# Kernel tuning notes

Measured on AMD Instinct MI355X. Metric: run time of the kernel, lower is better.

Reference implementation:

```python
import math
import jax, jax.numpy as jnp
import numpy as np

B, S, E = 2, 4096, 768
H, W = 12, 256  # num_heads, one-sided attention window
HD = E // H


def setup_inputs() -> dict:
    key = jax.random.key(0)
    ks = jax.random.split(key, 8)
    scale = 1.0 / math.sqrt(E)
    return {
        "hidden_states": jax.random.normal(ks[0], (B, S, E), jnp.float32),
        "attention_mask": jax.random.randint(ks[1], (B, 1, 1, S), 0, 2).astype(jnp.int32),
        "Wq": jax.random.normal(ks[2], (E, E), jnp.float32) * scale,
        "bq": jnp.zeros((E,), jnp.float32),
        "Wk": jax.random.normal(ks[3], (E, E), jnp.float32) * scale,
        "bk": jnp.zeros((E,), jnp.float32),
        "Wv": jax.random.normal(ks[4], (E, E), jnp.float32) * scale,
        "bv": jnp.zeros((E,), jnp.float32),
    }


def _to_heads(x, nc, w):
    # (B,S,E) -> (B*H, S, HD)
    return x.reshape(B, S, H, HD).transpose(0, 2, 1, 3).reshape(B * H, S, HD)


def _windows(x, nc, w):
    # (N, S, d) -> overlapping 3w key windows per query chunk: (N, nc, 3w, d)
    xp = jnp.pad(x, ((0, 0), (w, w), (0, 0))).reshape(x.shape[0], nc + 2, w, x.shape[-1])
    return jnp.concatenate([xp[:, :-2], xp[:, 1:-1], xp[:, 2:]], axis=2)


def reference(hidden_states, attention_mask, Wq, bq, Wk, bk, Wv, bv):
    w = W
    nc = S // w  # number of query chunks (seq_len % (2w) == 0)
    # Dense projections with relu activation (as in the source module)
    q = jax.nn.relu(hidden_states @ Wq + bq) / math.sqrt(HD)
    k = jax.nn.relu(hidden_states @ Wk + bk)
    v = jax.nn.relu(hidden_states @ Wv + bv)

    qc = _to_heads(q, nc, w).reshape(B * H, nc, w, HD)          # (BH, nc, w, d)
    kw = _windows(_to_heads(k, nc, w), nc, w)                    # (BH, nc, 3w, d)
    vw = _windows(_to_heads(v, nc, w), nc, w)                    # (BH, nc, 3w, d)

    # chunked QK^T: (BH, nc, w, 3w)
    scores = jnp.einsum('bcxd,bcyd->bcxy', qc, kw)

    rows = jnp.arange(w)[:, None]                                # (w,1)
    idx = rows + jnp.arange(2 * w + 1)[None, :]                  # (w, 2w+1) window column of diagonal j
    band = scores[:, :, rows, idx]                               # (BH, nc, w, 2w+1)

    # absolute key index of each band entry -> mask out-of-range diagonals
    abs_k = jnp.arange(nc)[:, None, None] * w + idx[None] - w    # (nc, w, 2w+1)
    valid = (abs_k >= 0) & (abs_k < S)

    # attention_mask != 0 -> add -10000 at those key positions within the band
    am = attention_mask.reshape(B, S)
    fm = jnp.where(am != 0, jnp.float32(-10000.0), jnp.float32(0.0))  # (B,S)
    fmp = jnp.pad(fm, ((0, 0), (w, w))).reshape(B, nc + 2, w)
    fmw = jnp.concatenate([fmp[:, :-2], fmp[:, 1:-1], fmp[:, 2:]], axis=2)  # (B, nc, 3w)
    fband = fmw[:, :, idx]                                       # (B, nc, w, 2w+1)

    band = band.reshape(B, H, nc, w, 2 * w + 1) + fband[:, None]
    band = jnp.where(valid, band, jnp.float32(-1e9))
    probs = jax.nn.softmax(band, axis=-1)                        # (B, H, nc, w, 2w+1)

    # chunked PV: scatter band back to (w, 3w) window layout, then matmul with v windows
    p = probs.reshape(B * H, nc, w, 2 * w + 1)
    pf = jnp.zeros((B * H, nc, w, 3 * w), p.dtype).at[:, :, rows, idx].set(p)
    attn = jnp.einsum('bcxy,bcyd->bcxd', pf, vw)                 # (BH, nc, w, d)
    attn = attn.reshape(B, H, S, HD).transpose(0, 2, 1, 3).reshape(B, S, E)

    probs_out = probs.reshape(B, H, S, 2 * w + 1).transpose(0, 2, 1, 3)  # (B,S,H,2w+1)
    return attn, probs_out
```

## Files before the change

kernel.cpp:

```cpp
#include <hip/hip_runtime.h>
#include <hip/hip_bf16.h>
#include <math.h>

#define Bsz 2
#define Ssz 4096
#define Esz 768
#define Hh 12
#define HDd 64
#define Ww 256
#define NBAND 513

typedef __attribute__((ext_vector_type(8))) short    bf16x8;
typedef __attribute__((ext_vector_type(8))) unsigned short us8;
typedef __attribute__((ext_vector_type(4))) float    f32x4;

#define WT_ELEMS (3*768*768)
#define QKV_BYTE_OFF ((size_t)2 * WT_ELEMS * 2)

__device__ inline unsigned short f2bf(float x) {
    unsigned int u = __float_as_uint(x);
    return (unsigned short)((u + 0x7fffu + ((u >> 16) & 1u)) >> 16);
}

__global__ __launch_bounds__(256) void cast_wt(
    const float* __restrict__ W0, const float* __restrict__ W1, const float* __restrict__ W2,
    unsigned short* __restrict__ wt_hi, unsigned short* __restrict__ wt_lo)
{
    const int z = blockIdx.z;
    const float* Wm = (z == 0) ? W0 : (z == 1) ? W1 : W2;
    __shared__ float tile[32][33];
    const int t = threadIdx.x;
    const int k0 = blockIdx.x * 32, n0 = blockIdx.y * 32;
    {
        int r = t >> 3, c = (t & 7) * 4;
        float4 v = *(const float4*)(Wm + (size_t)(k0 + r) * Esz + n0 + c);
        tile[r][c] = v.x; tile[r][c+1] = v.y; tile[r][c+2] = v.z; tile[r][c+3] = v.w;
    }
    __syncthreads();
    {
        int nr = t >> 3, c = (t & 7) * 4;
        unsigned short hb[4], lb[4];
        #pragma unroll
        for (int i = 0; i < 4; ++i) {
            float x = tile[c + i][nr];
            unsigned short h = f2bf(x);
            float hf = __uint_as_float((unsigned int)h << 16);
            hb[i] = h;
            lb[i] = f2bf(x - hf);
        }
        size_t off = ((size_t)z * Esz + n0 + nr) * Esz + k0 + c;
        *(ushort4*)(wt_hi + off) = make_ushort4(hb[0], hb[1], hb[2], hb[3]);
        *(ushort4*)(wt_lo + off) = make_ushort4(lb[0], lb[1], lb[2], lb[3]);
    }
}

#define BMg 128
#define BNg 128
#define BKg 32
#define LDT 40

__global__ __launch_bounds__(256) void qkv_gemm_mfma(
    const float* __restrict__ A,
    const unsigned short* __restrict__ wt_hi, const unsigned short* __restrict__ wt_lo,
    const float* __restrict__ b0, const float* __restrict__ b1, const float* __restrict__ b2,
    float* __restrict__ qkv)
{
    const int z = blockIdx.z;
    const float* bias = (z == 0) ? b0 : (z == 1) ? b1 : b2;
    const float scale = (z == 0) ? 0.125f : 1.0f;
    float* dst = qkv + (size_t)z * Bsz * Hh * Ssz * HDd;

    __shared__ unsigned short Ah[BMg][LDT], Al[BMg][LDT];
    __shared__ unsigned short Bh[BNg][LDT], Bl[BNg][LDT];

    const int t = threadIdx.x;
    const int row0 = blockIdx.y * BMg;
    const int col0 = blockIdx.x * BNg;
    const int wv = t >> 6, ln = t & 63;
    const int wm = wv >> 1, wn = wv & 1;
    const int fr = ln & 15, fc = ln >> 4;

    f32x4 acc[4][4] = {};

    const int sr = t >> 1;
    const int sk = (t & 1) * 16;

    const float* arow = A + (size_t)(row0 + sr) * Esz;
    const unsigned short* wth = wt_hi + ((size_t)z * Esz + col0 + sr) * Esz;
    const unsigned short* wtl = wt_lo + ((size_t)z * Esz + col0 + sr) * Esz;

    for (int k0 = 0; k0 < Esz; k0 += BKg) {
        {
            float4 v0 = *(const float4*)(arow + k0 + sk);
            float4 v1 = *(const float4*)(arow + k0 + sk + 4);
            float4 v2 = *(const float4*)(arow + k0 + sk + 8);
            float4 v3 = *(const float4*)(arow + k0 + sk + 12);
            float f[16] = {v0.x,v0.y,v0.z,v0.w, v1.x,v1.y,v1.z,v1.w,
                           v2.x,v2.y,v2.z,v2.w, v3.x,v3.y,v3.z,v3.w};
            us8 h0, h1, l0, l1;
            #pragma unroll
            for (int i = 0; i < 8; ++i) {
                unsigned short hb = f2bf(f[i]);
                h0[i] = hb;
                l0[i] = f2bf(f[i] - __uint_as_float((unsigned int)hb << 16));
            }
            #pragma unroll
            for (int i = 0; i < 8; ++i) {
                unsigned short hb = f2bf(f[8 + i]);
                h1[i] = hb;
                l1[i] = f2bf(f[8 + i] - __uint_as_float((unsigned int)hb << 16));
            }
            *(us8*)&Ah[sr][sk]     = h0;
            *(us8*)&Ah[sr][sk + 8] = h1;
            *(us8*)&Al[sr][sk]     = l0;
            *(us8*)&Al[sr][sk + 8] = l1;
        }
        {
            *(us8*)&Bh[sr][sk]     = *(const us8*)(wth + k0 + sk);
            *(us8*)&Bh[sr][sk + 8] = *(const us8*)(wth + k0 + sk + 8);
            *(us8*)&Bl[sr][sk]     = *(const us8*)(wtl + k0 + sk);
            *(us8*)&Bl[sr][sk + 8] = *(const us8*)(wtl + k0 + sk + 8);
        }
        __syncthreads();

        bf16x8 ah[4], al[4], bh[4], bl[4];
        #pragma unroll
        for (int m = 0; m < 4; ++m) {
            ah[m] = *(const bf16x8*)&Ah[wm * 64 + m * 16 + fr][fc * 8];
            al[m] = *(const bf16x8*)&Al[wm * 64 + m * 16 + fr][fc * 8];
        }
        #pragma unroll
        for (int n = 0; n < 4; ++n) {
            bh[n] = *(const bf16x8*)&Bh[wn * 64 + n * 16 + fr][fc * 8];
            bl[n] = *(const bf16x8*)&Bl[wn * 64 + n * 16 + fr][fc * 8];
        }
        #pragma unroll
        for (int m = 0; m < 4; ++m)
            #pragma unroll
            for (int n = 0; n < 4; ++n) {
                acc[m][n] = __builtin_amdgcn_mfma_f32_16x16x32_bf16(ah[m], bh[n], acc[m][n], 0, 0, 0);
                acc[m][n] = __builtin_amdgcn_mfma_f32_16x16x32_bf16(ah[m], bl[n], acc[m][n], 0, 0, 0);
                acc[m][n] = __builtin_amdgcn_mfma_f32_16x16x32_bf16(al[m], bh[n], acc[m][n], 0, 0, 0);
            }
        __syncthreads();
    }

    #pragma unroll
    for (int n = 0; n < 4; ++n) {
        int col = col0 + wn * 64 + n * 16 + fr;
        int h = col >> 6, d = col & 63;
        float bv = bias[col];
        #pragma unroll
        for (int m = 0; m < 4; ++m) {
            int rowb = row0 + wm * 64 + m * 16 + fc * 4;
            #pragma unroll
            for (int r = 0; r < 4; ++r) {
                int row = rowb + r;
                int b = row >> 12, s = row & 4095;
                float v = fmaxf(acc[m][n][r] + bv, 0.f) * scale;
                dst[(((size_t)b * Hh + h) * Ssz + s) * HDd + d] = v;
            }
        }
    }
}

#define ROWS 16
#define KT 64
#define NKT 9
#define LDKV 68
#define LDQ 68

__global__ __launch_bounds__(256) void attn_kernel(
    const float* __restrict__ ws, const int* __restrict__ am,
    float* __restrict__ out_attn, float* __restrict__ out_probs)
{
    const float* Qp = ws;
    const float* Kp = ws + (size_t)Bsz * Hh * Ssz * HDd;
    const float* Vp = Kp + (size_t)Bsz * Hh * Ssz * HDd;

    __shared__ float qs[ROWS][LDQ];
    __shared__ float kv[KT][LDKV];
    __shared__ float sc[ROWS][NBAND];

    const int tid = threadIdx.x;
    const int ngrp = Ssz / ROWS;
    const int bh = blockIdx.x / ngrp;
    const int rg = blockIdx.x % ngrp;
    const int b = bh / Hh, h = bh % Hh;
    const int s0 = rg * ROWS;

    for (int i = tid; i < ROWS * NBAND; i += 256) (&sc[0][0])[i] = -1e9f;

    {
        int xq = tid >> 4, d0 = (tid & 15) * 4;
        float4 qv = *(const float4*)(Qp + ((size_t)bh * Ssz + s0 + xq) * HDd + d0);
        *(float4*)&qs[xq][d0] = qv;
    }
    __syncthreads();

    const int x = tid >> 4;
    const int i16 = tid & 15;

    float qreg[HDd];
    #pragma unroll
    for (int d = 0; d < HDd; ++d) qreg[d] = qs[x][d];

    for (int kt = 0; kt < NKT; ++kt) {
        const int key0 = s0 - 256 + kt * 64;
        {
            int j = tid >> 2;
            int d0 = (tid & 3) * 16;
            int key = key0 + j;
            float4 r0 = {0,0,0,0}, r1 = r0, r2 = r0, r3 = r0;
            if (key >= 0 && key < Ssz) {
                const float4* src = (const float4*)(Kp + ((size_t)bh * Ssz + key) * HDd + d0);
                r0 = src[0]; r1 = src[1]; r2 = src[2]; r3 = src[3];
            }
            float4* dstp = (float4*)&kv[j][d0];
            dstp[0] = r0; dstp[1] = r1; dstp[2] = r2; dstp[3] = r3;
        }
        __syncthreads();
        #pragma unroll
        for (int a = 0; a < 4; ++a) {
            int j = i16 + a * 16;
            int key = key0 + j;
            int y = kt * 64 + j - x;
            if (key >= 0 && key < Ssz && y >= 0 && y <= 2 * Ww) {
                float dot = 0.f;
                #pragma unroll
                for (int t = 0; t < 16; ++t) {
                    float4 kk = *(const float4*)&kv[j][t * 4];
                    dot = fmaf(qreg[t*4+0], kk.x, dot);
                    dot = fmaf(qreg[t*4+1], kk.y, dot);
                    dot = fmaf(qreg[t*4+2], kk.z, dot);
                    dot = fmaf(qreg[t*4+3], kk.w, dot);
                }
                float fmv = (am[b * Ssz + key] != 0) ? -10000.f : 0.f;
                sc[x][y] = dot + fmv;
            }
        }
        __syncthreads();
    }

    {
        float m = -1e30f;
        for (int y = i16; y < NBAND; y += 16) m = fmaxf(m, sc[x][y]);
        m = fmaxf(m, __shfl_xor(m, 1));
        m = fmaxf(m, __shfl_xor(m, 2));
        m = fmaxf(m, __shfl_xor(m, 4));
        m = fmaxf(m, __shfl_xor(m, 8));
        float l = 0.f;
        for (int y = i16; y < NBAND; y += 16) {
            float e = __expf(sc[x][y] - m);
            sc[x][y] = e;
            l += e;
        }
        l += __shfl_xor(l, 1);
        l += __shfl_xor(l, 2);
        l += __shfl_xor(l, 4);
        l += __shfl_xor(l, 8);
        float rinv = 1.f / l;
        float* pbase = out_probs + ((size_t)(b * Ssz + s0 + x) * Hh + h) * NBAND;
        for (int y = i16; y < NBAND; y += 16) {
            float p = sc[x][y] * rinv;
            sc[x][y] = p;
            pbase[y] = p;
        }
    }
    __syncthreads();

    float4 acc = {0.f, 0.f, 0.f, 0.f};
    const int d0 = i16 * 4;
    for (int kt = 0; kt < NKT; ++kt) {
        const int key0 = s0 - 256 + kt * 64;
        {
            int j = tid >> 2;
            int dd = (tid & 3) * 16;
            int key = key0 + j;
            float4 r0 = {0,0,0,0}, r1 = r0, r2 = r0, r3 = r0;
            if (key >= 0 && key < Ssz) {
                const float4* src = (const float4*)(Vp + ((size_t)bh * Ssz + key) * HDd + dd);
                r0 = src[0]; r1 = src[1]; r2 = src[2]; r3 = src[3];
            }
            float4* dstp = (float4*)&kv[j][dd];
            dstp[0] = r0; dstp[1] = r1; dstp[2] = r2; dstp[3] = r3;
        }
        __syncthreads();
        for (int j = 0; j < KT; ++j) {
            int y = kt * 64 + j - x;
            if (y >= 0 && y <= 2 * Ww) {
                float p = sc[x][y];
                float4 vv = *(const float4*)&kv[j][d0];
                acc.x = fmaf(p, vv.x, acc.x);
                acc.y = fmaf(p, vv.y, acc.y);
                acc.z = fmaf(p, vv.z, acc.z);
                acc.w = fmaf(p, vv.w, acc.w);
            }
        }
        __syncthreads();
    }
    {
        float* obase = out_attn + ((size_t)b * Ssz + s0 + x) * Esz + h * HDd;
        *(float4*)&obase[d0] = acc;
    }
}

extern "C" void kernel_launch(void* const* d_in, const int* in_sizes, int n_in,
                              void* d_out, int out_size, void* d_ws, size_t ws_size,
                              hipStream_t stream)
{
    const float* hs = (const float*)d_in[0];
    const int*   am = (const int*)d_in[1];
    const float* Wq = (const float*)d_in[2];
    const float* bq = (const float*)d_in[3];
    const float* Wk = (const float*)d_in[4];
    const float* bk = (const float*)d_in[5];
    const float* Wv = (const float*)d_in[6];
    const float* bv = (const float*)d_in[7];

    unsigned short* wt_hi = (unsigned short*)d_ws;
    unsigned short* wt_lo = wt_hi + WT_ELEMS;
    float* qkv = (float*)((char*)d_ws + QKV_BYTE_OFF);

    float* out_attn  = (float*)d_out;
    float* out_probs = out_attn + (size_t)Bsz * Ssz * Esz;

    dim3 gc(24, 24, 3);
    cast_wt<<<gc, 256, 0, stream>>>(Wq, Wk, Wv, wt_hi, wt_lo);

    dim3 gg(Esz / BNg, (Bsz * Ssz) / BMg, 3);
    qkv_gemm_mfma<<<gg, 256, 0, stream>>>(hs, wt_hi, wt_lo, bq, bk, bv, qkv);

    dim3 g2(Bsz * Hh * (Ssz / ROWS));
    attn_kernel<<<g2, 256, 0, stream>>>(qkv, am, out_attn, out_probs);
}
```

Baseline: 892.9 us.

## Move banded attention QK and PV onto split-bf16 MFMA with transposed V

The scalar FP32 attention kernel is replaced by a single-wave MFMA kernel. Scores are computed with split hi/lo bf16 products (three-term) and softmax runs entirely in registers over 33 tiles of 16 keys, with P staged through small LDS tiles for the PV MFMA. The QKV GEMM now writes hi/lo bf16 halves instead of FP32, and a new kernel transposes V so PV B-operand loads are contiguous. This removes the heavy FP32 FMA and LDS traffic but adds an extra transpose pass and extra workspace. Each wave holds a large register array of scores, so occupancy may drop.

```diff
diff --git a/kernel.cpp b/kernel.cpp
--- a/kernel.cpp
+++ b/kernel.cpp
@@ -9,17 +9,21 @@
 #define HDd 64
 #define Ww 256
 #define NBAND 513
+#define BH (Bsz*Hh)
 
 typedef __attribute__((ext_vector_type(8))) short    bf16x8;
 typedef __attribute__((ext_vector_type(8))) unsigned short us8;
 typedef __attribute__((ext_vector_type(4))) float    f32x4;
 
 #define WT_ELEMS (3*768*768)
-#define QKV_BYTE_OFF ((size_t)2 * WT_ELEMS * 2)
+#define QKV_ELEMS ((size_t)BH * Ssz * HDd)
 
 __device__ inline unsigned short f2bf(float x) {
     unsigned int u = __float_as_uint(x);
     return (unsigned short)((u + 0x7fffu + ((u >> 16) & 1u)) >> 16);
+}
+__device__ inline float bf2f(unsigned short h) {
+    return __uint_as_float((unsigned int)h << 16);
 }
 
 __global__ __launch_bounds__(256) void cast_wt(
@@ -44,9 +48,8 @@
         for (int i = 0; i < 4; ++i) {
             float x = tile[c + i][nr];
             unsigned short h = f2bf(x);
-            float hf = __uint_as_float((unsigned int)h << 16);
             hb[i] = h;
-            lb[i] = f2bf(x - hf);
+            lb[i] = f2bf(x - bf2f(h));
         }
         size_t off = ((size_t)z * Esz + n0 + nr) * Esz + k0 + c;
         *(ushort4*)(wt_hi + off) = make_ushort4(hb[0], hb[1], hb[2], hb[3]);
@@ -63,12 +66,13 @@
     const float* __restrict__ A,
     const unsigned short* __restrict__ wt_hi, const unsigned short* __restrict__ wt_lo,
     const float* __restrict__ b0, const float* __restrict__ b1, const float* __restrict__ b2,
-    float* __restrict__ qkv)
+    unsigned short* __restrict__ qkvb)
 {
     const int z = blockIdx.z;
     const float* bias = (z == 0) ? b0 : (z == 1) ? b1 : b2;
     const float scale = (z == 0) ? 0.125f : 1.0f;
-    float* dst = qkv + (size_t)z * Bsz * Hh * Ssz * HDd;
+    unsigned short* zh = qkvb + (size_t)z * 2 * QKV_ELEMS;
+    unsigned short* zl = zh + QKV_ELEMS;
 
     __shared__ unsigned short Ah[BMg][LDT], Al[BMg][LDT];
     __shared__ unsigned short Bh[BNg][LDT], Bl[BNg][LDT];
@@ -102,13 +106,13 @@
             for (int i = 0; i < 8; ++i) {
                 unsigned short hb = f2bf(f[i]);
                 h0[i] = hb;
-                l0[i] = f2bf(f[i] - __uint_as_float((unsigned int)hb << 16));
+                l0[i] = f2bf(f[i] - bf2f(hb));
             }
             #pragma unroll
             for (int i = 0; i < 8; ++i) {
                 unsigned short hb = f2bf(f[8 + i]);
                 h1[i] = hb;
-                l1[i] = f2bf(f[8 + i] - __uint_as_float((unsigned int)hb << 16));
+                l1[i] = f2bf(f[8 + i] - bf2f(hb));
             }
             *(us8*)&Ah[sr][sk]     = h0;
             *(us8*)&Ah[sr][sk + 8] = h1;
@@ -158,150 +162,192 @@
                 int row = rowb + r;
                 int b = row >> 12, s = row & 4095;
                 float v = fmaxf(acc[m][n][r] + bv, 0.f) * scale;
-                dst[(((size_t)b * Hh + h) * Ssz + s) * HDd + d] = v;
-            }
-        }
-    }
-}
-
-#define ROWS 16
-#define KT 64
-#define NKT 9
-#define LDKV 68
-#define LDQ 68
-
-__global__ __launch_bounds__(256) void attn_kernel(
-    const float* __restrict__ ws, const int* __restrict__ am,
+                unsigned short hv = f2bf(v);
+                unsigned short lv = f2bf(v - bf2f(hv));
+                size_t idx = (((size_t)b * Hh + h) * Ssz + s) * HDd + d;
+                zh[idx] = hv;
+                zl[idx] = lv;
+            }
+        }
+    }
+}
+
+__global__ __launch_bounds__(256) void transpose_v(
+    const unsigned short* __restrict__ vh, const unsigned short* __restrict__ vl,
+    unsigned short* __restrict__ vth, unsigned short* __restrict__ vtl)
+{
+    __shared__ unsigned short tile[64][72];
+    const int z = blockIdx.z;
+    const unsigned short* src = z ? vl : vh;
+    unsigned short*       dst = z ? vtl : vth;
+    const int bh = blockIdx.y;
+    const int st = blockIdx.x;
+    const int t = threadIdx.x;
+    {
+        int sr = t >> 2, dc = (t & 3) * 16;
+        const unsigned short* sp = src + ((size_t)bh * Ssz + st * 64 + sr) * HDd + dc;
+        *(us8*)&tile[sr][dc]     = *(const us8*)sp;
+        *(us8*)&tile[sr][dc + 8] = *(const us8*)(sp + 8);
+    }
+    __syncthreads();
+    {
+        int dr = t >> 2, sc = (t & 3) * 16;
+        us8 b0, b1;
+        #pragma unroll
+        for (int j = 0; j < 8; ++j) b0[j] = tile[sc + j][dr];
+        #pragma unroll
+        for (int j = 0; j < 8; ++j) b1[j] = tile[sc + 8 + j][dr];
+        unsigned short* dp = dst + ((size_t)bh * HDd + dr) * Ssz + st * 64 + sc;
+        *(us8*)dp       = b0;
+        *(us8*)(dp + 8) = b1;
+    }
+}
+
+__global__ __launch_bounds__(64) void attn_mfma(
+    const unsigned short* __restrict__ Qh, const unsigned short* __restrict__ Ql,
+    const unsigned short* __restrict__ Kh, const unsigned short* __restrict__ Kl,
+    const unsigned short* __restrict__ Vth, const unsigned short* __restrict__ Vtl,
+    const int* __restrict__ am,
     float* __restrict__ out_attn, float* __restrict__ out_probs)
 {
-    const float* Qp = ws;
-    const float* Kp = ws + (size_t)Bsz * Hh * Ssz * HDd;
-    const float* Vp = Kp + (size_t)Bsz * Hh * Ssz * HDd;
-
-    __shared__ float qs[ROWS][LDQ];
-    __shared__ float kv[KT][LDKV];
-    __shared__ float sc[ROWS][NBAND];
-
-    const int tid = threadIdx.x;
-    const int ngrp = Ssz / ROWS;
-    const int bh = blockIdx.x / ngrp;
-    const int rg = blockIdx.x % ngrp;
+    __shared__ unsigned short Ph[16][32], Pl[16][32];
+
+    const int blk = blockIdx.x;
+    const int qg = blk & 255;
+    const int bh = blk >> 8;
     const int b = bh / Hh, h = bh % Hh;
-    const int s0 = rg * ROWS;
-
-    for (int i = tid; i < ROWS * NBAND; i += 256) (&sc[0][0])[i] = -1e9f;
-
-    {
-        int xq = tid >> 4, d0 = (tid & 15) * 4;
-        float4 qv = *(const float4*)(Qp + ((size_t)bh * Ssz + s0 + xq) * HDd + d0);
-        *(float4*)&qs[xq][d0] = qv;
-    }
-    __syncthreads();
-
-    const int x = tid >> 4;
-    const int i16 = tid & 15;
-
-    float qreg[HDd];
-    #pragma unroll
-    for (int d = 0; d < HDd; ++d) qreg[d] = qs[x][d];
-
-    for (int kt = 0; kt < NKT; ++kt) {
-        const int key0 = s0 - 256 + kt * 64;
-        {
-            int j = tid >> 2;
-            int d0 = (tid & 3) * 16;
-            int key = key0 + j;
-            float4 r0 = {0,0,0,0}, r1 = r0, r2 = r0, r3 = r0;
-            if (key >= 0 && key < Ssz) {
-                const float4* src = (const float4*)(Kp + ((size_t)bh * Ssz + key) * HDd + d0);
-                r0 = src[0]; r1 = src[1]; r2 = src[2]; r3 = src[3];
-            }
-            float4* dstp = (float4*)&kv[j][d0];
-            dstp[0] = r0; dstp[1] = r1; dstp[2] = r2; dstp[3] = r3;
-        }
-        __syncthreads();
-        #pragma unroll
-        for (int a = 0; a < 4; ++a) {
-            int j = i16 + a * 16;
-            int key = key0 + j;
-            int y = kt * 64 + j - x;
-            if (key >= 0 && key < Ssz && y >= 0 && y <= 2 * Ww) {
-                float dot = 0.f;
-                #pragma unroll
-                for (int t = 0; t < 16; ++t) {
-                    float4 kk = *(const float4*)&kv[j][t * 4];
-                    dot = fmaf(qreg[t*4+0], kk.x, dot);
-                    dot = fmaf(qreg[t*4+1], kk.y, dot);
-                    dot = fmaf(qreg[t*4+2], kk.z, dot);
-                    dot = fmaf(qreg[t*4+3], kk.w, dot);
-                }
-                float fmv = (am[b * Ssz + key] != 0) ? -10000.f : 0.f;
-                sc[x][y] = dot + fmv;
-            }
-        }
-        __syncthreads();
-    }
-
-    {
-        float m = -1e30f;
-        for (int y = i16; y < NBAND; y += 16) m = fmaxf(m, sc[x][y]);
+    const int s0w = qg * 16;
+    const int ln = threadIdx.x;
+    const int col = ln & 15;
+    const int grp = ln >> 4;
+
+    const size_t qbase = ((size_t)bh * Ssz + s0w + col) * HDd + grp * 8;
+    const bf16x8 q_h0 = *(const bf16x8*)(Qh + qbase);
+    const bf16x8 q_h1 = *(const bf16x8*)(Qh + qbase + 32);
+    const bf16x8 q_l0 = *(const bf16x8*)(Ql + qbase);
+    const bf16x8 q_l1 = *(const bf16x8*)(Ql + qbase + 32);
+
+    f32x4 sS[33];
+    const int key0base = s0w - 256;
+    #pragma unroll
+    for (int t = 0; t < 33; ++t) {
+        int key = key0base + 16 * t + col;
+        int keyc = min(max(key, 0), Ssz - 1);
+        const size_t kb = ((size_t)bh * Ssz + keyc) * HDd + grp * 8;
+        bf16x8 k_h0 = *(const bf16x8*)(Kh + kb);
+        bf16x8 k_h1 = *(const bf16x8*)(Kh + kb + 32);
+        bf16x8 k_l0 = *(const bf16x8*)(Kl + kb);
+        bf16x8 k_l1 = *(const bf16x8*)(Kl + kb + 32);
+        f32x4 s = {};
+        s = __builtin_amdgcn_mfma_f32_16x16x32_bf16(q_h0, k_h0, s, 0, 0, 0);
+        s = __builtin_amdgcn_mfma_f32_16x16x32_bf16(q_h1, k_h1, s, 0, 0, 0);
+        s = __builtin_amdgcn_mfma_f32_16x16x32_bf16(q_h0, k_l0, s, 0, 0, 0);
+        s = __builtin_amdgcn_mfma_f32_16x16x32_bf16(q_h1, k_l1, s, 0, 0, 0);
+        s = __builtin_amdgcn_mfma_f32_16x16x32_bf16(q_l0, k_h0, s, 0, 0, 0);
+        s = __builtin_amdgcn_mfma_f32_16x16x32_bf16(q_l1, k_h1, s, 0, 0, 0);
+        float fm = (am[b * Ssz + keyc] != 0) ? -10000.f : 0.f;
+        bool keyok = (key >= 0) && (key < Ssz);
+        #pragma unroll
+        for (int r = 0; r < 4; ++r) {
+            int x = grp * 4 + r;
+            int yy = 16 * t + col - x;
+            bool valid = keyok && (yy >= 0) && (yy <= 512);
+            s[r] = valid ? (s[r] + fm) : -1e9f;
+        }
+        sS[t] = s;
+    }
+
+    float mrow[4], lrow[4];
+    #pragma unroll
+    for (int r = 0; r < 4; ++r) {
+        float m = sS[0][r];
+        #pragma unroll
+        for (int t = 1; t < 33; ++t) m = fmaxf(m, sS[t][r]);
         m = fmaxf(m, __shfl_xor(m, 1));
         m = fmaxf(m, __shfl_xor(m, 2));
         m = fmaxf(m, __shfl_xor(m, 4));
         m = fmaxf(m, __shfl_xor(m, 8));
+        mrow[r] = m;
+    }
+    #pragma unroll
+    for (int t = 0; t < 33; ++t)
+        #pragma unroll
+        for (int r = 0; r < 4; ++r)
+            sS[t][r] = __expf(sS[t][r] - mrow[r]);
+    #pragma unroll
+    for (int r = 0; r < 4; ++r) {
         float l = 0.f;
-        for (int y = i16; y < NBAND; y += 16) {
-            float e = __expf(sc[x][y] - m);
-            sc[x][y] = e;
-            l += e;
-        }
+        #pragma unroll
+        for (int t = 0; t < 33; ++t) l += sS[t][r];
         l += __shfl_xor(l, 1);
         l += __shfl_xor(l, 2);
         l += __shfl_xor(l, 4);
         l += __shfl_xor(l, 8);
-        float rinv = 1.f / l;
-        float* pbase = out_probs + ((size_t)(b * Ssz + s0 + x) * Hh + h) * NBAND;
-        for (int y = i16; y < NBAND; y += 16) {
-            float p = sc[x][y] * rinv;
-            sc[x][y] = p;
-            pbase[y] = p;
-        }
-    }
-    __syncthreads();
-
-    float4 acc = {0.f, 0.f, 0.f, 0.f};
-    const int d0 = i16 * 4;
-    for (int kt = 0; kt < NKT; ++kt) {
-        const int key0 = s0 - 256 + kt * 64;
-        {
-            int j = tid >> 2;
-            int dd = (tid & 3) * 16;
-            int key = key0 + j;
-            float4 r0 = {0,0,0,0}, r1 = r0, r2 = r0, r3 = r0;
-            if (key >= 0 && key < Ssz) {
-                const float4* src = (const float4*)(Vp + ((size_t)bh * Ssz + key) * HDd + dd);
-                r0 = src[0]; r1 = src[1]; r2 = src[2]; r3 = src[3];
-            }
-            float4* dstp = (float4*)&kv[j][dd];
-            dstp[0] = r0; dstp[1] = r1; dstp[2] = r2; dstp[3] = r3;
-        }
+        lrow[r] = 1.f / l;
+    }
+
+    #pragma unroll
+    for (int t = 0; t < 33; ++t) {
+        #pragma unroll
+        for (int r = 0; r < 4; ++r) {
+            float p = sS[t][r] * lrow[r];
+            sS[t][r] = p;
+            int x = grp * 4 + r;
+            int yy = 16 * t + col - x;
+            if (yy >= 0 && yy <= 512) {
+                out_probs[(((size_t)b * Ssz + s0w + x) * Hh + h) * NBAND + yy] = p;
+            }
+        }
+    }
+
+    f32x4 acc[4] = {};
+    #pragma unroll
+    for (int pp = 0; pp < 17; ++pp) {
         __syncthreads();
-        for (int j = 0; j < KT; ++j) {
-            int y = kt * 64 + j - x;
-            if (y >= 0 && y <= 2 * Ww) {
-                float p = sc[x][y];
-                float4 vv = *(const float4*)&kv[j][d0];
-                acc.x = fmaf(p, vv.x, acc.x);
-                acc.y = fmaf(p, vv.y, acc.y);
-                acc.z = fmaf(p, vv.z, acc.z);
-                acc.w = fmaf(p, vv.w, acc.w);
+        #pragma unroll
+        for (int tt = 0; tt < 2; ++tt) {
+            const int t = 2 * pp + tt;
+            if (t < 33) {
+                #pragma unroll
+                for (int r = 0; r < 4; ++r) {
+                    float p = sS[t][r];
+                    unsigned short hp = f2bf(p);
+                    unsigned short lp = f2bf(p - bf2f(hp));
+                    Ph[grp * 4 + r][tt * 16 + col] = hp;
+                    Pl[grp * 4 + r][tt * 16 + col] = lp;
+                }
+            } else {
+                #pragma unroll
+                for (int r = 0; r < 4; ++r) {
+                    Ph[grp * 4 + r][tt * 16 + col] = 0;
+                    Pl[grp * 4 + r][tt * 16 + col] = 0;
+                }
             }
         }
         __syncthreads();
-    }
-    {
-        float* obase = out_attn + ((size_t)b * Ssz + s0 + x) * Esz + h * HDd;
-        *(float4*)&obase[d0] = acc;
+        bf16x8 pah = *(const bf16x8*)&Ph[col][grp * 8];
+        bf16x8 pal = *(const bf16x8*)&Pl[col][grp * 8];
+        int kbase = s0w - 256 + 32 * pp + grp * 8;
+        int kc = min(max(kbase, 0), Ssz - 8);
+        #pragma unroll
+        for (int dt = 0; dt < 4; ++dt) {
+            const size_t vb = ((size_t)bh * HDd + dt * 16 + col) * Ssz + kc;
+            bf16x8 v_h = *(const bf16x8*)(Vth + vb);
+            bf16x8 v_l = *(const bf16x8*)(Vtl + vb);
+            acc[dt] = __builtin_amdgcn_mfma_f32_16x16x32_bf16(pah, v_h, acc[dt], 0, 0, 0);
+            acc[dt] = __builtin_amdgcn_mfma_f32_16x16x32_bf16(pah, v_l, acc[dt], 0, 0, 0);
+            acc[dt] = __builtin_amdgcn_mfma_f32_16x16x32_bf16(pal, v_h, acc[dt], 0, 0, 0);
+        }
+    }
+
+    #pragma unroll
+    for (int dt = 0; dt < 4; ++dt) {
+        #pragma unroll
+        for (int r = 0; r < 4; ++r) {
+            int x = grp * 4 + r;
+            int d = dt * 16 + col;
+            out_attn[((size_t)b * Ssz + s0w + x) * Esz + h * HDd + d] = acc[dt][r];
+        }
     }
 }
 
@@ -320,7 +366,15 @@
 
     unsigned short* wt_hi = (unsigned short*)d_ws;
     unsigned short* wt_lo = wt_hi + WT_ELEMS;
-    float* qkv = (float*)((char*)d_ws + QKV_BYTE_OFF);
+    unsigned short* qkvb  = wt_lo + WT_ELEMS;
+    unsigned short* qh  = qkvb;
+    unsigned short* ql  = qh + QKV_ELEMS;
+    unsigned short* kh  = ql + QKV_ELEMS;
+    unsigned short* kl  = kh + QKV_ELEMS;
+    unsigned short* vh  = kl + QKV_ELEMS;
+    unsigned short* vl  = vh + QKV_ELEMS;
+    unsigned short* vth = vl + QKV_ELEMS;
+    unsigned short* vtl = vth + QKV_ELEMS;
 
     float* out_attn  = (float*)d_out;
     float* out_probs = out_attn + (size_t)Bsz * Ssz * Esz;
@@ -329,8 +383,11 @@
     cast_wt<<<gc, 256, 0, stream>>>(Wq, Wk, Wv, wt_hi, wt_lo);
 
     dim3 gg(Esz / BNg, (Bsz * Ssz) / BMg, 3);
-    qkv_gemm_mfma<<<gg, 256, 0, stream>>>(hs, wt_hi, wt_lo, bq, bk, bv, qkv);
-
-    dim3 g2(Bsz * Hh * (Ssz / ROWS));
-    attn_kernel<<<g2, 256, 0, stream>>>(qkv, am, out_attn, out_probs);
-}
+    qkv_gemm_mfma<<<gg, 256, 0, stream>>>(hs, wt_hi, wt_lo, bq, bk, bv, qkvb);
+
+    dim3 gt(Ssz / 64, BH, 2);
+    transpose_v<<<gt, 256, 0, stream>>>(vh, vl, vth, vtl);
+
+    dim3 ga(BH * (Ssz / 16));
+    attn_mfma<<<ga, 64, 0, stream>>>(qh, ql, kh, kl, vth, vtl, am, out_attn, out_probs);
+}
```

Result: faster. 724.5 us (-18.9%).
